# Kernel optimization log

Hardware: AMD Instinct MI355X
Metric: run time of the kernel (lower is better)

## Reference

```python
import jax, jax.numpy as jnp
import numpy as np

N_NODES = 100000


def _gcn_norm(edge_index, num_nodes):
    # PyG GCNConv default: add self-loops, symmetric normalization
    src, dst = edge_index[0], edge_index[1]
    loop = jnp.arange(num_nodes, dtype=src.dtype)
    src = jnp.concatenate([src, loop])
    dst = jnp.concatenate([dst, loop])
    deg = jax.ops.segment_sum(jnp.ones_like(dst, dtype=jnp.float32), dst,
                              num_segments=num_nodes)
    dinv = jnp.where(deg > 0, jax.lax.rsqrt(deg), 0.0)
    norm = dinv[src] * dinv[dst]  # [E + N]
    return src, dst, norm


def _gcn_conv(x, W, b, src, dst, norm, num_nodes):
    h = x @ W                                   # [N, out] linear first (PyG)
    msg = h[src] * norm[:, None]                # gather + scale  [E+N, out]
    out = jax.ops.segment_sum(msg, dst, num_segments=num_nodes)  # scatter-add
    return out + b


def setup_inputs() -> dict:
    key = jax.random.key(0)
    ks = jax.random.split(key, 5)
    x = jax.random.normal(ks[0], (N_NODES, 3), dtype=jnp.float32)
    edge_index = jax.random.randint(ks[1], (2, 1600000), 0, N_NODES, dtype=jnp.int64)
    # Glorot-ish weights, zero bias (PyG defaults)
    W1 = jax.random.normal(ks[2], (3, 64), dtype=jnp.float32) * (1.0 / np.sqrt(3))
    W2 = jax.random.normal(ks[3], (64, 64), dtype=jnp.float32) * (1.0 / np.sqrt(64))
    W3 = jax.random.normal(ks[4], (64, 3), dtype=jnp.float32) * (1.0 / np.sqrt(64))
    b1 = jnp.zeros((64,), jnp.float32)
    b2 = jnp.zeros((64,), jnp.float32)
    b3 = jnp.zeros((3,), jnp.float32)
    return {"x": x, "edge_index": edge_index, "W1": W1, "b1": b1,
            "W2": W2, "b2": b2, "W3": W3, "b3": b3}


def reference(x, edge_index, W1, b1, W2, b2, W3, b3):
    n = x.shape[0]
    src, dst, norm = _gcn_norm(edge_index, n)  # same graph for every layer
    h = jax.nn.relu(_gcn_conv(x, W1, b1, src, dst, norm, n))
    h = jax.nn.relu(_gcn_conv(h, W2, b2, src, dst, norm, n))
    return _gcn_conv(h, W3, b3, src, dst, norm, n)
```

## Files before the change

### kernel.cpp

```cpp
#include <hip/hip_runtime.h>

#define TPB 256
#define NB 391
#define CH 4096
#define BS 4736


__device__ __forceinline__ unsigned bpack(float a, float b) {
    unsigned ua = __float_as_uint(a), ub = __float_as_uint(b);
    ua = (ua + 0x7fffu + ((ua >> 16) & 1u)) >> 16;
    ub = (ub + 0x7fffu + ((ub >> 16) & 1u)) >> 16;
    return ua | (ub << 16);
}
__device__ __forceinline__ float blo(unsigned u) { return __uint_as_float(u << 16); }
__device__ __forceinline__ float bhi(unsigned u) { return __uint_as_float(u & 0xffff0000u); }


__global__ __launch_bounds__(TPB) void k_placeA(const int* __restrict__ src,
                                                const int* __restrict__ dst,
                                                unsigned* __restrict__ gcur,
                                                unsigned* __restrict__ bkt, int E) {
    __shared__ unsigned val[CH];
    __shared__ unsigned dstS[CH];
    __shared__ unsigned short bid[CH];
    __shared__ unsigned cnt[512], loff[512], lcur[512], basev[512];
    __shared__ unsigned tsum[TPB];
    int t = threadIdx.x;
    int c0 = blockIdx.x * CH;
    int n = E - c0; if (n > CH) n = CH;

    for (int b = t; b < 512; b += TPB) { cnt[b] = 0; lcur[b] = 0; }
    __syncthreads();
    for (int i = t; i < n; i += TPB) {
        unsigned d = (unsigned)dst[c0 + i];
        dstS[i] = d;
        atomicAdd(&cnt[d >> 8], 1u);
    }
    __syncthreads();
    for (int b = t; b < NB; b += TPB)
        basev[b] = cnt[b] ? atomicAdd(&gcur[b], cnt[b]) : 0u;
    unsigned a0 = cnt[2 * t], a1 = cnt[2 * t + 1];
    tsum[t] = a0 + a1;
    __syncthreads();
#pragma unroll
    for (int o = 1; o < TPB; o <<= 1) {
        unsigned v = (t >= o) ? tsum[t - o] : 0u;
        __syncthreads();
        tsum[t] += v;
        __syncthreads();
    }
    unsigned ex = tsum[t] - (a0 + a1);
    loff[2 * t] = ex; loff[2 * t + 1] = ex + a0;
    __syncthreads();
    for (int i = t; i < n; i += TPB) {
        unsigned s = (unsigned)src[c0 + i];
        unsigned d = dstS[i];
        unsigned b = d >> 8;
        unsigned r = atomicAdd(&lcur[b], 1u);
        unsigned slot = loff[b] + r;
        val[slot] = s | ((d & 255u) << 20);
        bid[slot] = (unsigned short)b;
    }
    __syncthreads();
    for (int i = t; i < n; i += TPB) {
        unsigned b = bid[i];
        bkt[(size_t)b * BS + basev[b] + ((unsigned)i - loff[b])] = val[i];
    }
}


__global__ __launch_bounds__(512) void k_fineS(const unsigned* __restrict__ bkt,
                                               const unsigned* __restrict__ gcur,
                                               const float* __restrict__ x,
                                               int2* __restrict__ rp2,
                                               int* __restrict__ ssrc,
                                               float* __restrict__ dinv,
                                               float4* __restrict__ xs4, int N) {
    __shared__ unsigned cnt[256], sc[256], off[256];
    __shared__ unsigned bs[BS];
    int t = threadIdx.x, b = blockIdx.x;
    if (t < 256) cnt[t] = 0;
    __syncthreads();
    int p0 = b * BS;
    int n = (int)gcur[b];
    for (int i = t; i < n; i += 512) {
        unsigned u = bkt[p0 + i];
        bs[i] = u;
        atomicAdd(&cnt[u >> 20], 1u);
    }
    __syncthreads();
    unsigned c = (t < 256) ? cnt[t] : 0u;
    if (t < 256) sc[t] = c;
    __syncthreads();
#pragma unroll
    for (int o = 1; o < 256; o <<= 1) {
        unsigned v = (t >= o && t < 256) ? sc[t - o] : 0u;
        __syncthreads();
        if (t < 256) sc[t] += v;
        __syncthreads();
    }
    if (t < 256) {
        unsigned ex = sc[t] - c;
        off[t] = (unsigned)p0 + ex;
        int node = (b << 8) + t;
        if (node < N) {
            int beg = p0 + (int)ex;
            rp2[node] = make_int2(beg, beg + (int)c);
            float dv = rsqrtf((float)(c + 1u));
            dinv[node] = dv;
            float4 xv;
            xv.x = x[node * 3 + 0] * dv;
            xv.y = x[node * 3 + 1] * dv;
            xv.z = x[node * 3 + 2] * dv;
            xv.w = 0.f;
            xs4[node] = xv;
        }
    }
    __syncthreads();
    for (int i = t; i < n; i += 512) {
        unsigned u = bs[i];
        unsigned r = atomicAdd(&off[u >> 20], 1u);
        ssrc[r] = (int)(u & 0xFFFFFu);
    }
}


__global__ __launch_bounds__(TPB) void k_l1q(const float* __restrict__ xs4,
                                             const int2* __restrict__ rp2,
                                             const int* __restrict__ ssrc,
                                             const float* __restrict__ dinv,
                                             const float* __restrict__ W1,
                                             const float* __restrict__ b1,
                                             const float* __restrict__ W2,
                                             uint4* __restrict__ gb, int N) {
    __shared__ float Ws[4096];
    for (int i = threadIdx.x; i < 4096; i += TPB) Ws[i] = W2[i];
    __syncthreads();
    int tid = blockIdx.x * TPB + threadIdx.x;
    int node = tid >> 2, c = tid & 3;
    if (node >= N) return;
    int2 r = rp2[node];
    float acc = xs4[tid];
    int j = r.x;
    for (; j + 3 < r.y; j += 4) {
        int s0 = ssrc[j], s1 = ssrc[j+1], s2 = ssrc[j+2], s3 = ssrc[j+3];
        acc += (xs4[(s0 << 2) + c] + xs4[(s1 << 2) + c])
             + (xs4[(s2 << 2) + c] + xs4[(s3 << 2) + c]);
    }
    for (; j < r.y; ++j) acc += xs4[(ssrc[j] << 2) + c];
    float dv = dinv[node];
    acc *= dv;
    int base = (threadIdx.x & 63) & ~3;
    float q0 = __shfl(acc, base + 0, 64);
    float q1 = __shfl(acc, base + 1, 64);
    float q2 = __shfl(acc, base + 2, 64);

    float o[16];
#pragma unroll
    for (int i = 0; i < 16; ++i) o[i] = 0.f;
    const int cofs = c << 4;
    for (int kb = 0; kb < 16; ++kb) {
        int k0 = __builtin_amdgcn_readfirstlane(kb) << 2;
        const float* W1k = W1 + k0;
        const float* b1k = b1 + k0;
        float h[4];
        h[0] = fmaxf(fmaf(q0, W1k[0], fmaf(q1, W1k[64], fmaf(q2, W1k[128], b1k[0]))), 0.f);
        h[1] = fmaxf(fmaf(q0, W1k[1], fmaf(q1, W1k[65], fmaf(q2, W1k[129], b1k[1]))), 0.f);
        h[2] = fmaxf(fmaf(q0, W1k[2], fmaf(q1, W1k[66], fmaf(q2, W1k[130], b1k[2]))), 0.f);
        h[3] = fmaxf(fmaf(q0, W1k[3], fmaf(q1, W1k[67], fmaf(q2, W1k[131], b1k[3]))), 0.f);
#pragma unroll
        for (int kk = 0; kk < 4; ++kk) {
            const float4* Wp = (const float4*)(Ws + ((k0 + kk) << 6) + cofs);
#pragma unroll
            for (int ii = 0; ii < 4; ++ii) {
                float4 w = Wp[ii];
                o[4*ii+0] = fmaf(h[kk], w.x, o[4*ii+0]);
                o[4*ii+1] = fmaf(h[kk], w.y, o[4*ii+1]);
                o[4*ii+2] = fmaf(h[kk], w.z, o[4*ii+2]);
                o[4*ii+3] = fmaf(h[kk], w.w, o[4*ii+3]);
            }
        }
    }
    uint4 v0, v1;
    v0.x = bpack(o[0] * dv,  o[1] * dv);
    v0.y = bpack(o[2] * dv,  o[3] * dv);
    v0.z = bpack(o[4] * dv,  o[5] * dv);
    v0.w = bpack(o[6] * dv,  o[7] * dv);
    v1.x = bpack(o[8] * dv,  o[9] * dv);
    v1.y = bpack(o[10] * dv, o[11] * dv);
    v1.z = bpack(o[12] * dv, o[13] * dv);
    v1.w = bpack(o[14] * dv, o[15] * dv);
    uint4* gp = gb + ((size_t)node << 3) + (c << 1);
    gp[0] = v0;
    gp[1] = v1;
}


__global__ __launch_bounds__(TPB) void k_p2fb(const uint4* __restrict__ gb,
                                              const int2* __restrict__ rp2,
                                              const int* __restrict__ ssrc,
                                              const float* __restrict__ dinv,
                                              const float* __restrict__ b2,
                                              const float* __restrict__ W3,
                                              float* __restrict__ q4, int N) {
    int tid = blockIdx.x * TPB + threadIdx.x;
    int node = tid >> 3, q = tid & 7;
    if (node >= N) return;
    int2 r = rp2[node];
    int beg = r.x, end = r.y;
    float a[8];
    {
        uint4 u = gb[((size_t)node << 3) + q];
        a[0] = blo(u.x); a[1] = bhi(u.x);
        a[2] = blo(u.y); a[3] = bhi(u.y);
        a[4] = blo(u.z); a[5] = bhi(u.z);
        a[6] = blo(u.w); a[7] = bhi(u.w);
    }
    int j = beg;
    for (; j + 3 < end; j += 4) {
        int s0 = ssrc[j], s1 = ssrc[j+1], s2 = ssrc[j+2], s3 = ssrc[j+3];
        uint4 u0 = gb[((size_t)s0 << 3) + q];
        uint4 u1 = gb[((size_t)s1 << 3) + q];
        uint4 u2 = gb[((size_t)s2 << 3) + q];
        uint4 u3 = gb[((size_t)s3 << 3) + q];
        a[0] += (blo(u0.x) + blo(u1.x)) + (blo(u2.x) + blo(u3.x));
        a[1] += (bhi(u0.x) + bhi(u1.x)) + (bhi(u2.x) + bhi(u3.x));
        a[2] += (blo(u0.y) + blo(u1.y)) + (blo(u2.y) + blo(u3.y));
        a[3] += (bhi(u0.y) + bhi(u1.y)) + (bhi(u2.y) + bhi(u3.y));
        a[4] += (blo(u0.z) + blo(u1.z)) + (blo(u2.z) + blo(u3.z));
        a[5] += (bhi(u0.z) + bhi(u1.z)) + (bhi(u2.z) + bhi(u3.z));
        a[6] += (blo(u0.w) + blo(u1.w)) + (blo(u2.w) + blo(u3.w));
        a[7] += (bhi(u0.w) + bhi(u1.w)) + (bhi(u2.w) + bhi(u3.w));
    }
    for (; j < end; ++j) {
        uint4 u = gb[((size_t)ssrc[j] << 3) + q];
        a[0] += blo(u.x); a[1] += bhi(u.x);
        a[2] += blo(u.y); a[3] += bhi(u.y);
        a[4] += blo(u.z); a[5] += bhi(u.z);
        a[6] += blo(u.w); a[7] += bhi(u.w);
    }
    float dv = dinv[node];
    int f0 = q << 3;
    const float* bb = b2 + f0;
    const float* Wr = W3 + f0 * 3;
    float p0 = 0.f, p1 = 0.f, p2 = 0.f;
#pragma unroll
    for (int i = 0; i < 8; ++i) {
        float h = fmaxf(fmaf(a[i], dv, bb[i]), 0.f);
        p0 = fmaf(h, Wr[3*i+0], p0);
        p1 = fmaf(h, Wr[3*i+1], p1);
        p2 = fmaf(h, Wr[3*i+2], p2);
    }
#pragma unroll
    for (int off = 1; off < 8; off <<= 1) {
        p0 += __shfl_xor(p0, off, 64);
        p1 += __shfl_xor(p1, off, 64);
        p2 += __shfl_xor(p2, off, 64);
    }
    if (q < 4) {
        float v = (q == 0) ? p0 * dv : (q == 1) ? p1 * dv : (q == 2) ? p2 * dv : 0.f;
        q4[((size_t)node << 2) + q] = v;
    }
}


__global__ __launch_bounds__(TPB) void k_pull3o(const float* __restrict__ g34,
                                                const int2* __restrict__ rp2,
                                                const int* __restrict__ ssrc,
                                                const float* __restrict__ dinv,
                                                const float* __restrict__ b3,
                                                float* __restrict__ out, int N) {
    int tid = blockIdx.x * TPB + threadIdx.x;
    int node = tid >> 2, c = tid & 3;
    if (node >= N) return;
    int2 r = rp2[node];
    int beg = r.x, end = r.y;
    float acc = g34[tid];
    int j = beg;
    for (; j + 3 < end; j += 4) {
        int s0 = ssrc[j], s1 = ssrc[j+1], s2 = ssrc[j+2], s3 = ssrc[j+3];
        acc += (g34[(s0 << 2) + c] + g34[(s1 << 2) + c])
             + (g34[(s2 << 2) + c] + g34[(s3 << 2) + c]);
    }
    for (; j < end; ++j) acc += g34[(ssrc[j] << 2) + c];
    if (c < 3) out[(size_t)node * 3 + c] = dinv[node] * acc + b3[c];
}

extern "C" void kernel_launch(void* const* d_in, const int* in_sizes, int n_in,
                              void* d_out, int out_size, void* d_ws, size_t ws_size,
                              hipStream_t stream) {
    const float* x  = (const float*)d_in[0];
    const int*   ei = (const int*)  d_in[1];
    const float* W1 = (const float*)d_in[2];
    const float* b1 = (const float*)d_in[3];
    const float* W2 = (const float*)d_in[4];
    const float* b2 = (const float*)d_in[5];
    const float* W3 = (const float*)d_in[6];
    const float* b3 = (const float*)d_in[7];
    float* out = (float*)d_out;

    const int N = in_sizes[0] / 3;
    const int E = in_sizes[1] / 2;
    const int* srcI = ei;
    const int* dstI = ei + E;

    float*    ws   = (float*)d_ws;
    unsigned* gcur = (unsigned*)ws;
    int2*     rp2  = (int2*)    (ws + 512);
    float*    dinv = ws + 512 + 2 * (size_t)N;
    int*      ssrc = (int*)     (dinv + N);
    float*    xs4  = (float*)(ssrc + (size_t)NB * BS + 4);
    float*    q4   = xs4 + (size_t)N * 4;
    unsigned* gb   = (unsigned*)(q4 + (size_t)N * 4);
    unsigned* bkt  = gb + (size_t)N * 32;

    int gPlace = (E + CH - 1) / CH;
    int gS3    = (N * 4 + TPB - 1) / TPB;
    int gP2    = (int)(((size_t)N * 8 + TPB - 1) / TPB);

    hipMemsetAsync(gcur, 0, 512 * sizeof(unsigned), stream);
    k_placeA<<<gPlace, TPB, 0, stream>>>(srcI, dstI, gcur, bkt, E);
    k_fineS <<<NB,     512, 0, stream>>>(bkt, gcur, x, rp2, ssrc, dinv,
                                         (float4*)xs4, N);

    k_l1q<<<gS3, TPB, 0, stream>>>(xs4, rp2, ssrc, dinv,
                                   W1, b1, W2, (uint4*)gb, N);

    k_p2fb<<<gP2, TPB, 0, stream>>>((const uint4*)gb, rp2, ssrc, dinv,
                                    b2, W3, q4, N);

    k_pull3o<<<gS3, TPB, 0, stream>>>(q4, rp2, ssrc, dinv, b3, out, N);
}
```

Measured before the change: 209.1 us.

## Sort edges by source sub-bin within each destination and pack W2 as bf16

The fine CSR build now counts edges into 2048 bins, keyed by destination node plus the top bits of the source index, and prefix-sums across them. Each node's neighbor list therefore comes out roughly sorted by source, which should make the later gathers more local. Separately, the layer-1 kernel stores W2 in shared memory as packed bf16, halving LDS footprint and load traffic. This costs a larger scan and extra unpack ALU work, and rounding W2 to bf16 lowers precision.

```diff
diff --git a/kernel.cpp b/kernel.cpp
--- a/kernel.cpp
+++ b/kernel.cpp
@@ -76,35 +76,49 @@
                                                int* __restrict__ ssrc,
                                                float* __restrict__ dinv,
                                                float4* __restrict__ xs4, int N) {
-    __shared__ unsigned cnt[256], sc[256], off[256];
+    __shared__ unsigned bins[2048];
+    __shared__ unsigned tsum[512];
+    __shared__ unsigned degS[256];
     __shared__ unsigned bs[BS];
     int t = threadIdx.x, b = blockIdx.x;
-    if (t < 256) cnt[t] = 0;
+    for (int i = t; i < 2048; i += 512) bins[i] = 0;
     __syncthreads();
     int p0 = b * BS;
     int n = (int)gcur[b];
     for (int i = t; i < n; i += 512) {
         unsigned u = bkt[p0 + i];
         bs[i] = u;
-        atomicAdd(&cnt[u >> 20], 1u);
-    }
-    __syncthreads();
-    unsigned c = (t < 256) ? cnt[t] : 0u;
-    if (t < 256) sc[t] = c;
-    __syncthreads();
-#pragma unroll
-    for (int o = 1; o < 256; o <<= 1) {
-        unsigned v = (t >= o && t < 256) ? sc[t - o] : 0u;
+        unsigned bin = ((u >> 20) << 3) | ((u & 0xFFFFFu) >> 14);
+        atomicAdd(&bins[bin], 1u);
+    }
+    __syncthreads();
+    unsigned s0 = bins[4*t], s1 = bins[4*t+1], s2 = bins[4*t+2], s3 = bins[4*t+3];
+    if (t < 256) {
+        unsigned s = 0;
+#pragma unroll
+        for (int i = 0; i < 8; ++i) s += bins[(t << 3) + i];
+        degS[t] = s;
+    }
+    __syncthreads();
+    unsigned e1 = s0, e2 = s0 + s1, e3 = e2 + s2;
+    unsigned tot = e3 + s3;
+    tsum[t] = tot;
+    __syncthreads();
+#pragma unroll
+    for (int o = 1; o < 512; o <<= 1) {
+        unsigned v = (t >= o) ? tsum[t - o] : 0u;
         __syncthreads();
-        if (t < 256) sc[t] += v;
+        tsum[t] += v;
         __syncthreads();
     }
+    unsigned ex = tsum[t] - tot;
+    bins[4*t] = ex; bins[4*t+1] = ex + e1; bins[4*t+2] = ex + e2; bins[4*t+3] = ex + e3;
+    __syncthreads();
     if (t < 256) {
-        unsigned ex = sc[t] - c;
-        off[t] = (unsigned)p0 + ex;
         int node = (b << 8) + t;
         if (node < N) {
-            int beg = p0 + (int)ex;
+            unsigned c = degS[t];
+            int beg = p0 + (int)bins[t << 3];
             rp2[node] = make_int2(beg, beg + (int)c);
             float dv = rsqrtf((float)(c + 1u));
             dinv[node] = dv;
@@ -119,8 +133,9 @@
     __syncthreads();
     for (int i = t; i < n; i += 512) {
         unsigned u = bs[i];
-        unsigned r = atomicAdd(&off[u >> 20], 1u);
-        ssrc[r] = (int)(u & 0xFFFFFu);
+        unsigned bin = ((u >> 20) << 3) | ((u & 0xFFFFFu) >> 14);
+        unsigned r = atomicAdd(&bins[bin], 1u);
+        ssrc[p0 + (int)r] = (int)(u & 0xFFFFFu);
     }
 }
 
@@ -133,8 +148,9 @@
                                              const float* __restrict__ b1,
                                              const float* __restrict__ W2,
                                              uint4* __restrict__ gb, int N) {
-    __shared__ float Ws[4096];
-    for (int i = threadIdx.x; i < 4096; i += TPB) Ws[i] = W2[i];
+    __shared__ unsigned Ws2[2048];
+    for (int i = threadIdx.x; i < 2048; i += TPB)
+        Ws2[i] = bpack(W2[2 * i], W2[2 * i + 1]);
     __syncthreads();
     int tid = blockIdx.x * TPB + threadIdx.x;
     int node = tid >> 2, c = tid & 3;
@@ -158,7 +174,7 @@
     float o[16];
 #pragma unroll
     for (int i = 0; i < 16; ++i) o[i] = 0.f;
-    const int cofs = c << 4;
+    const int cofs8 = c << 3;
     for (int kb = 0; kb < 16; ++kb) {
         int k0 = __builtin_amdgcn_readfirstlane(kb) << 2;
         const float* W1k = W1 + k0;
@@ -170,15 +186,18 @@
         h[3] = fmaxf(fmaf(q0, W1k[3], fmaf(q1, W1k[67], fmaf(q2, W1k[131], b1k[3]))), 0.f);
 #pragma unroll
         for (int kk = 0; kk < 4; ++kk) {
-            const float4* Wp = (const float4*)(Ws + ((k0 + kk) << 6) + cofs);
-#pragma unroll
-            for (int ii = 0; ii < 4; ++ii) {
-                float4 w = Wp[ii];
-                o[4*ii+0] = fmaf(h[kk], w.x, o[4*ii+0]);
-                o[4*ii+1] = fmaf(h[kk], w.y, o[4*ii+1]);
-                o[4*ii+2] = fmaf(h[kk], w.z, o[4*ii+2]);
-                o[4*ii+3] = fmaf(h[kk], w.w, o[4*ii+3]);
-            }
+            const uint4* Wp = (const uint4*)(Ws2 + ((k0 + kk) << 5) + cofs8);
+            uint4 wA = Wp[0];
+            uint4 wB = Wp[1];
+            float hv = h[kk];
+            o[0]  = fmaf(hv, blo(wA.x), o[0]);  o[1]  = fmaf(hv, bhi(wA.x), o[1]);
+            o[2]  = fmaf(hv, blo(wA.y), o[2]);  o[3]  = fmaf(hv, bhi(wA.y), o[3]);
+            o[4]  = fmaf(hv, blo(wA.z), o[4]);  o[5]  = fmaf(hv, bhi(wA.z), o[5]);
+            o[6]  = fmaf(hv, blo(wA.w), o[6]);  o[7]  = fmaf(hv, bhi(wA.w), o[7]);
+            o[8]  = fmaf(hv, blo(wB.x), o[8]);  o[9]  = fmaf(hv, bhi(wB.x), o[9]);
+            o[10] = fmaf(hv, blo(wB.y), o[10]); o[11] = fmaf(hv, bhi(wB.y), o[11]);
+            o[12] = fmaf(hv, blo(wB.z), o[12]); o[13] = fmaf(hv, bhi(wB.z), o[13]);
+            o[14] = fmaf(hv, blo(wB.w), o[14]); o[15] = fmaf(hv, bhi(wB.w), o[15]);
         }
     }
     uint4 v0, v1;
```

Measured after the change: 206.9 us. About the same (-1.1%).
